# Kernel tuning notes

Measured on AMD Instinct MI355X. Metric: run time of the kernel, lower is better.

The kernel has to match this reference:

```python
import jax, jax.numpy as jnp
import numpy as np

EPS = 1e-5

def _ln(x, g, b):
    mu = jnp.mean(x, axis=-1, keepdims=True)
    var = jnp.mean(jnp.square(x - mu), axis=-1, keepdims=True)
    return (x - mu) * jax.lax.rsqrt(var + EPS) * g + b

def setup_inputs() -> dict:
    key = jax.random.key(0)
    ks = jax.random.split(key, 16)
    B, L, D, H = 1, 512, 128, 128  # d_pair=128, d_hidden=128
    s_d = 1.0 / np.sqrt(D)
    s_h = 1.0 / np.sqrt(H)
    return {
        "pair": jax.random.normal(ks[0], (B, L, L, D), jnp.float32),
        "ln_g": jnp.ones((D,), jnp.float32),
        "ln_b": jnp.zeros((D,), jnp.float32),
        "lw": jax.random.normal(ks[1], (H, D), jnp.float32) * s_d,
        "lb": jnp.zeros((H,), jnp.float32),
        "lgw": jax.random.normal(ks[2], (H, D), jnp.float32) * s_d,
        "lgb": jnp.ones((H,), jnp.float32),
        "rw": jax.random.normal(ks[3], (H, D), jnp.float32) * s_d,
        "rb": jnp.zeros((H,), jnp.float32),
        "rgw": jax.random.normal(ks[4], (H, D), jnp.float32) * s_d,
        "rgb": jnp.ones((H,), jnp.float32),
        "gw": jax.random.normal(ks[5], (D, D), jnp.float32) * s_d,
        "gb": jnp.ones((D,), jnp.float32),
        "lno_g": jnp.ones((H,), jnp.float32),
        "lno_b": jnp.zeros((H,), jnp.float32),
        "ow": jax.random.normal(ks[6], (D, H), jnp.float32) * s_h,
        "ob": jnp.zeros((D,), jnp.float32),
    }

def reference(pair, ln_g, ln_b, lw, lb, lgw, lgb, rw, rb, rgw, rgb, gw, gb, lno_g, lno_b, ow, ob):
    L = pair.shape[1]
    p = _ln(pair, ln_g, ln_b)                                   # [B,L,L,D]
    left = jax.nn.sigmoid(p @ lgw.T + lgb) * (p @ lw.T + lb)    # [B,L,L,H]
    right = jax.nn.sigmoid(p @ rgw.T + rgb) * (p @ rw.T + rb)   # [B,L,L,H]
    # outgoing: contract over k (second seq dim)
    out = jnp.einsum('bikd,bjkd->bijd', left, right / jnp.float32(L))
    out = _ln(out, lno_g, lno_b)
    out = out @ ow.T + ob                                       # [B,L,L,D]
    gate = jax.nn.sigmoid(p @ gw.T + gb)
    return gate * out
```

## Files before the change

kernel.cpp:

```cpp
#include <hip/hip_runtime.h>
#include <hip/hip_bf16.h>
#include <stdint.h>

#define LSEQ 512
#define LL   262144

typedef __attribute__((ext_vector_type(8))) short short8;
typedef __attribute__((ext_vector_type(4))) float f32x4;
typedef __attribute__((ext_vector_type(4))) unsigned short us4;
typedef __attribute__((ext_vector_type(8))) unsigned short us8;

static_assert(sizeof(short8) == 16, "");
static_assert(sizeof(us8) == 16, "");

__device__ inline unsigned short f2bf(float f){
  unsigned u = __builtin_bit_cast(unsigned, f);
  unsigned r = (u + 0x7fffu + ((u >> 16) & 1u)) >> 16;
  return (unsigned short)r;
}
__device__ inline float bf2f(unsigned short s){
  return __builtin_bit_cast(float, ((unsigned)s) << 16);
}
__device__ inline float sigm(float x){ return 1.f / (1.f + __expf(-x)); }

__device__ inline int sw256(int row, int byte_in_row){
  return row*256 + ((((byte_in_row >> 4) ^ (row & 7))) << 4) + (byte_in_row & 15);
}
__device__ inline int sw128(int row, int byte_in_row){
  return row*128 + ((((byte_in_row >> 4) ^ (row & 7))) << 4) + (byte_in_row & 15);
}

__device__ inline void gload16(const void* g, void* lds){
  __builtin_amdgcn_global_load_lds(
      (const __attribute__((address_space(1))) unsigned*)g,
      (__attribute__((address_space(3))) unsigned*)lds, 16, 0, 0);
}

__global__ __launch_bounds__(128) void k0_prep(
    const float* __restrict__ lw, const float* __restrict__ lgw,
    const float* __restrict__ rw, const float* __restrict__ rgw,
    const float* __restrict__ gw, const float* __restrict__ ow,
    const float* __restrict__ lnog, const float* __restrict__ lnob,
    const float* __restrict__ ob,
    unsigned short* __restrict__ wbf, float* __restrict__ swg, float* __restrict__ swb)
{
  const int dd = blockIdx.x;
  const int t  = threadIdx.x;
  const int idx = dd*128 + t;
  wbf[0*16384 + idx] = f2bf(lgw[idx]);
  wbf[1*16384 + idx] = f2bf(lw[idx]);
  wbf[2*16384 + idx] = f2bf(rgw[idx]);
  wbf[3*16384 + idx] = f2bf(rw[idx]);
  wbf[4*16384 + idx] = f2bf(gw[idx]);
  float o = ow[idx];
  float a = o * lnog[t];
  float b = o * lnob[t];
  wbf[5*16384 + idx] = f2bf(a);
  #pragma unroll
  for (int m = 1; m < 64; m <<= 1){ a += __shfl_xor(a, m); b += __shfl_xor(b, m); }
  __shared__ float sA[2], sB[2];
  if ((t & 63) == 0){ sA[t >> 6] = a; sB[t >> 6] = b; }
  __syncthreads();
  if (t == 0){ swg[dd] = sA[0] + sA[1]; swb[dd] = sB[0] + sB[1] + ob[dd]; }
}

__global__ __launch_bounds__(256) void k1_proj(
    const float* __restrict__ pair, const float* __restrict__ ln_g, const float* __restrict__ ln_b,
    const float* __restrict__ lb,  const float* __restrict__ lgb,
    const float* __restrict__ rb,  const float* __restrict__ rgb,
    const float* __restrict__ gb,
    const unsigned short* __restrict__ wbf,
    unsigned short* __restrict__ lt, unsigned short* __restrict__ rt,
    unsigned short* __restrict__ gate)
{
  __shared__ char p_l[32768];
  __shared__ char wb_l[32768];
  const int t = threadIdx.x;
  const int b = blockIdx.x;
  const int w = t >> 6, l = t & 63;
  const long pos0 = (long)(b >> 2)*512 + (long)(b & 3)*128;

  {
    const int col = (t & 31) * 4;
    const float4 g4 = *(const float4*)(ln_g + col);
    const float4 b4 = *(const float4*)(ln_b + col);
    #pragma unroll 4
    for (int pass = 0; pass < 16; ++pass){
      const int row = pass*8 + (t >> 5);
      const float4 x = *(const float4*)(pair + (pos0 + row)*128 + col);
      float s = x.x + x.y + x.z + x.w;
      float q = x.x*x.x + x.y*x.y + x.z*x.z + x.w*x.w;
      #pragma unroll
      for (int m = 1; m < 32; m <<= 1){ s += __shfl_xor(s, m); q += __shfl_xor(q, m); }
      const float mu = s * (1.f/128.f);
      const float rs = rsqrtf(q * (1.f/128.f) - mu*mu + 1e-5f);
      us4 o;
      o.x = f2bf((x.x - mu)*rs*g4.x + b4.x);
      o.y = f2bf((x.y - mu)*rs*g4.y + b4.y);
      o.z = f2bf((x.z - mu)*rs*g4.z + b4.z);
      o.w = f2bf((x.w - mu)*rs*g4.w + b4.w);
      *(us4*)(p_l + sw256(row, col*2)) = o;
    }
  }
  __syncthreads();

  auto stageW = [&](int wi){
    const char* ws = (const char*)(wbf + wi*16384);
    #pragma unroll
    for (int q = 0; q < 8; ++q){
      int P = q*4096 + t*16;
      gload16(ws + sw256(P >> 8, P & 255), wb_l + P);
    }
  };

  auto zero2 = [&](f32x4 (&a)[2][8]){
    #pragma unroll
    for (int m = 0; m < 2; ++m)
      #pragma unroll
      for (int n = 0; n < 8; ++n) a[m][n] = f32x4{0.f,0.f,0.f,0.f};
  };

  auto gemm = [&](f32x4 (&acc)[2][8]){
    #pragma unroll
    for (int ks = 0; ks < 4; ++ks){
      short8 a[2];
      #pragma unroll
      for (int m = 0; m < 2; ++m){
        int row = w*32 + m*16 + (l & 15);
        a[m] = *(const short8*)(p_l + sw256(row, ks*64 + (l >> 4)*16));
      }
      #pragma unroll
      for (int n = 0; n < 8; ++n){
        int row = n*16 + (l & 15);
        short8 bb = *(const short8*)(wb_l + sw256(row, ks*64 + (l >> 4)*16));
        #pragma unroll
        for (int m = 0; m < 2; ++m)
          acc[m][n] = __builtin_amdgcn_mfma_f32_16x16x32_bf16(a[m], bb, acc[m][n], 0, 0, 0);
      }
    }
  };

  auto combineWrite = [&](f32x4 (&aG)[2][8], f32x4 (&aL)[2][8],
                          const float* gbias, const float* lbias, unsigned short* dst){
    float gv[8], lv[8];
    #pragma unroll
    for (int n = 0; n < 8; ++n){ gv[n] = gbias[n*16 + (l & 15)]; lv[n] = lbias[n*16 + (l & 15)]; }
    __syncthreads();
    #pragma unroll
    for (int m = 0; m < 2; ++m){
      #pragma unroll
      for (int n = 0; n < 8; ++n){
        us4 o;
        #pragma unroll
        for (int r = 0; r < 4; ++r)
          o[r] = f2bf(sigm(aG[m][n][r] + gv[n]) * (aL[m][n][r] + lv[n]));
        int h  = n*16 + (l & 15);
        int r0 = w*32 + m*16 + (l >> 4)*4;
        *(us4*)(wb_l + sw256(h, r0*2)) = o;
      }
    }
    __syncthreads();
    #pragma unroll
    for (int it = 0; it < 8; ++it){
      int hh = it*16 + (t >> 4), ch = t & 15;
      us8 v = *(const us8*)(wb_l + sw256(hh, ch*16));
      *(us8*)(dst + (long)hh*LL + pos0 + ch*8) = v;
    }
    __syncthreads();
  };

  f32x4 aG[2][8], aL[2][8];

  zero2(aG); zero2(aL);
  stageW(0); __syncthreads(); gemm(aG); __syncthreads();
  stageW(1); __syncthreads(); gemm(aL);
  combineWrite(aG, aL, lgb, lb, lt);

  zero2(aG); zero2(aL);
  stageW(2); __syncthreads(); gemm(aG); __syncthreads();
  stageW(3); __syncthreads(); gemm(aL);
  combineWrite(aG, aL, rgb, rb, rt);

  zero2(aG);
  stageW(4); __syncthreads(); gemm(aG);
  {
    float gv[8];
    #pragma unroll
    for (int n = 0; n < 8; ++n) gv[n] = gb[n*16 + (l & 15)];
    __syncthreads();
    #pragma unroll
    for (int m = 0; m < 2; ++m)
      #pragma unroll
      for (int n = 0; n < 8; ++n)
        #pragma unroll
        for (int r = 0; r < 4; ++r){
          int row = w*32 + m*16 + (l >> 4)*4 + r;
          int h   = n*16 + (l & 15);
          *(unsigned short*)(wb_l + sw256(row, h*2)) = f2bf(sigm(aG[m][n][r] + gv[n]));
        }
    __syncthreads();
    #pragma unroll
    for (int it = 0; it < 8; ++it){
      int row = it*16 + (t >> 4), ch = t & 15;
      us8 v = *(const us8*)(wb_l + sw256(row, ch*16));
      *(us8*)(gate + (pos0 + row)*128 + ch*8) = v;
    }
  }
}

__global__ __launch_bounds__(256) void k2_tri(
    const unsigned short* __restrict__ lt, const unsigned short* __restrict__ rt,
    unsigned short* __restrict__ omm)
{
  __shared__ char smem[32768];
  char* As = smem;
  char* Bs = smem + 16384;
  const int t = threadIdx.x, b = blockIdx.x;
  const int d = b & 127, tile = b >> 7;
  const int i0 = (tile >> 2)*128, j0 = (tile & 3)*128;
  const unsigned short* Ag = lt + (long)d*LL;
  const unsigned short* Bg = rt + (long)d*LL;
  const int w = t >> 6, l = t & 63;
  const int wm = w >> 1, wn = w & 1;

  f32x4 acc[4][4];
  #pragma unroll
  for (int m = 0; m < 4; ++m)
    #pragma unroll
    for (int n = 0; n < 4; ++n) acc[m][n] = f32x4{0.f,0.f,0.f,0.f};

  for (int kt = 0; kt < 8; ++kt){
    const int k0 = kt*64;
    __syncthreads();
    #pragma unroll
    for (int q = 0; q < 4; ++q){
      int P = q*4096 + t*16;
      int row = P >> 7;
      int ls  = ((P >> 4) & 7) ^ (row & 7);
      gload16(Ag + (long)(i0 + row)*512 + k0 + ls*8, As + P);
      gload16(Bg + (long)(j0 + row)*512 + k0 + ls*8, Bs + P);
    }
    __syncthreads();
    #pragma unroll
    for (int ks = 0; ks < 2; ++ks){
      short8 a[4], bb[4];
      #pragma unroll
      for (int m = 0; m < 4; ++m){
        int row = wm*64 + m*16 + (l & 15);
        a[m] = *(const short8*)(As + sw128(row, ks*64 + (l >> 4)*16));
      }
      #pragma unroll
      for (int n = 0; n < 4; ++n){
        int row = wn*64 + n*16 + (l & 15);
        bb[n] = *(const short8*)(Bs + sw128(row, ks*64 + (l >> 4)*16));
      }
      #pragma unroll
      for (int m = 0; m < 4; ++m)
        #pragma unroll
        for (int n = 0; n < 4; ++n)
          acc[m][n] = __builtin_amdgcn_mfma_f32_16x16x32_bf16(a[m], bb[n], acc[m][n], 0, 0, 0);
    }
  }
  __syncthreads();
  #pragma unroll
  for (int m = 0; m < 4; ++m)
    #pragma unroll
    for (int n = 0; n < 4; ++n)
      #pragma unroll
      for (int r = 0; r < 4; ++r){
        int row = wm*64 + m*16 + (l >> 4)*4 + r;
        int j   = wn*64 + n*16 + (l & 15);
        *(unsigned short*)(smem + sw256(row, j*2)) = f2bf(acc[m][n][r] * (1.f/512.f));
      }
  __syncthreads();
  #pragma unroll
  for (int it = 0; it < 8; ++it){
    int row = it*16 + (t >> 4), ch = t & 15;
    us8 v = *(const us8*)(smem + sw256(row, ch*16));
    *(us8*)(omm + (long)d*LL + (long)(i0 + row)*512 + j0 + ch*8) = v;
  }
}

__global__ __launch_bounds__(256) void k3_out(
    const unsigned short* __restrict__ omm, const unsigned short* __restrict__ gate,
    const unsigned short* __restrict__ wgbf,
    const float* __restrict__ swg, const float* __restrict__ swb,
    float* __restrict__ out)
{
  __shared__ char omm_l[32768];
  __shared__ char wg_l[32768];
  __shared__ float mu_s[128], rs_s[128];
  const int t = threadIdx.x;
  const int jt = blockIdx.x, i = blockIdx.y;
  const int j0 = jt*128;
  const int w = t >> 6, l = t & 63;

  {
    const int jc = t & 15, dg = t >> 4;
    float sum[8], sq[8];
    #pragma unroll
    for (int e = 0; e < 8; ++e){ sum[e] = 0.f; sq[e] = 0.f; }
    #pragma unroll
    for (int q = 0; q < 8; ++q){
      int dd = dg + q*16;
      us8 v = *(const us8*)(omm + (long)dd*LL + (long)i*512 + j0 + jc*8);
      *(us8*)(omm_l + dd*256 + jc*16) = v;
      #pragma unroll
      for (int e = 0; e < 8; ++e){
        float f = bf2f(v[e]);
        sum[e] += f; sq[e] += f*f;
      }
    }
    float* scr = (float*)wg_l;
    #pragma unroll
    for (int e = 0; e < 8; ++e){
      scr[dg*128 + jc*8 + e]        = sum[e];
      scr[2048 + dg*128 + jc*8 + e] = sq[e];
    }
  }
  __syncthreads();
  if (t < 128){
    const float* scr = (const float*)wg_l;
    float s1 = 0.f, s2 = 0.f;
    #pragma unroll
    for (int g = 0; g < 16; ++g){ s1 += scr[g*128 + t]; s2 += scr[2048 + g*128 + t]; }
    float mu = s1 * (1.f/128.f);
    float var = s2 * (1.f/128.f) - mu*mu;
    mu_s[t] = mu;
    rs_s[t] = rsqrtf(var + 1e-5f);
  }
  __syncthreads();
  #pragma unroll
  for (int q = 0; q < 8; ++q){
    int P = q*4096 + t*16;
    gload16((const char*)wgbf + sw256(P >> 8, P & 255), wg_l + P);
  }
  __syncthreads();

  f32x4 acc[2][8];
  #pragma unroll
  for (int m = 0; m < 2; ++m)
    #pragma unroll
    for (int n = 0; n < 8; ++n) acc[m][n] = f32x4{0.f,0.f,0.f,0.f};

  #pragma unroll
  for (int ks = 0; ks < 4; ++ks){
    short8 a[2];
    #pragma unroll
    for (int m = 0; m < 2; ++m){
      const int jj = w*32 + m*16 + (l & 15);
      short8 av;
      #pragma unroll
      for (int e = 0; e < 8; ++e){
        int dd = ks*32 + (l >> 4)*8 + e;
        av[e] = *(const short*)(omm_l + dd*256 + jj*2);
      }
      a[m] = av;
    }
    #pragma unroll
    for (int n = 0; n < 8; ++n){
      int row = n*16 + (l & 15);
      short8 bb = *(const short8*)(wg_l + sw256(row, ks*64 + (l >> 4)*16));
      #pragma unroll
      for (int m = 0; m < 2; ++m)
        acc[m][n] = __builtin_amdgcn_mfma_f32_16x16x32_bf16(a[m], bb, acc[m][n], 0, 0, 0);
    }
  }

  float swgv[8], swbv[8];
  #pragma unroll
  for (int n = 0; n < 8; ++n){ swgv[n] = swg[n*16 + (l & 15)]; swbv[n] = swb[n*16 + (l & 15)]; }
  #pragma unroll
  for (int m = 0; m < 2; ++m){
    #pragma unroll
    for (int r = 0; r < 4; ++r){
      int j = w*32 + m*16 + (l >> 4)*4 + r;
      float mu = mu_s[j], rs = rs_s[j];
      long rowoff = ((long)i*512 + j0 + j)*128;
      #pragma unroll
      for (int n = 0; n < 8; ++n){
        int ddx = n*16 + (l & 15);
        float val = rs*(acc[m][n][r] - mu*swgv[n]) + swbv[n];
        out[rowoff + ddx] = val * bf2f(gate[rowoff + ddx]);
      }
    }
  }
}

extern "C" void kernel_launch(void* const* d_in, const int* in_sizes, int n_in,
                              void* d_out, int out_size, void* d_ws, size_t ws_size,
                              hipStream_t stream)
{
  const float* pair = (const float*)d_in[0];
  const float* ln_g = (const float*)d_in[1];
  const float* ln_b = (const float*)d_in[2];
  const float* lw   = (const float*)d_in[3];
  const float* lb   = (const float*)d_in[4];
  const float* lgw  = (const float*)d_in[5];
  const float* lgb  = (const float*)d_in[6];
  const float* rw   = (const float*)d_in[7];
  const float* rb   = (const float*)d_in[8];
  const float* rgw  = (const float*)d_in[9];
  const float* rgb  = (const float*)d_in[10];
  const float* gw   = (const float*)d_in[11];
  const float* gb   = (const float*)d_in[12];
  const float* lnog = (const float*)d_in[13];
  const float* lnob = (const float*)d_in[14];
  const float* ow   = (const float*)d_in[15];
  const float* ob   = (const float*)d_in[16];
  float* out = (float*)d_out;

  char* ws = (char*)d_ws;
  unsigned short* lt   = (unsigned short*)(ws);
  unsigned short* rt   = (unsigned short*)(ws + (1l << 26));
  unsigned short* gate = (unsigned short*)(ws + (2l << 26));
  unsigned short* omm  = (unsigned short*)(ws + (3l << 26));
  unsigned short* wbf  = (unsigned short*)(ws + (4l << 26));
  float* swg = (float*)(ws + (4l << 26) + 196608);
  float* swb = swg + 128;

  k0_prep<<<dim3(128), dim3(128), 0, stream>>>(lw, lgw, rw, rgw, gw, ow, lnog, lnob, ob,
                                               wbf, swg, swb);
  k1_proj<<<dim3(2048), dim3(256), 0, stream>>>(pair, ln_g, ln_b, lb, lgb, rb, rgb, gb,
                                                wbf, lt, rt, gate);
  k2_tri<<<dim3(2048), dim3(256), 0, stream>>>(lt, rt, omm);
  k3_out<<<dim3(4, 512), dim3(256), 0, stream>>>(omm, gate, wbf + 5*16384, swg, swb, out);
}
```

Before: 341.1 us.

## Pre-pack projection weights in MFMA fragment order and halve k1 tile size

Adds a pack kernel that lays out the five projection weight matrices in per-lane MFMA B-fragment order, so k1 loads them straight from global into registers instead of staging them through LDS. k1 now processes 64 rows per block and keeps the A fragments resident in registers. Each wave owns a slice of output columns and computes the gate and linear arms together. LDS use is halved and launch bounds request 3 blocks per CU to raise occupancy. The packed weights live in the omm workspace region, which k2 overwrites only later. The trade-off is that weights are re-read from global/L2 by every block, and there is more register pressure from holding the A fragments.

```diff
diff --git a/kernel.cpp b/kernel.cpp
--- a/kernel.cpp
+++ b/kernel.cpp
@@ -37,25 +37,17 @@
 }
 
 __global__ __launch_bounds__(128) void k0_prep(
-    const float* __restrict__ lw, const float* __restrict__ lgw,
-    const float* __restrict__ rw, const float* __restrict__ rgw,
-    const float* __restrict__ gw, const float* __restrict__ ow,
-    const float* __restrict__ lnog, const float* __restrict__ lnob,
-    const float* __restrict__ ob,
-    unsigned short* __restrict__ wbf, float* __restrict__ swg, float* __restrict__ swb)
+    const float* __restrict__ ow, const float* __restrict__ lnog,
+    const float* __restrict__ lnob, const float* __restrict__ ob,
+    unsigned short* __restrict__ wgbf, float* __restrict__ swg, float* __restrict__ swb)
 {
   const int dd = blockIdx.x;
   const int t  = threadIdx.x;
   const int idx = dd*128 + t;
-  wbf[0*16384 + idx] = f2bf(lgw[idx]);
-  wbf[1*16384 + idx] = f2bf(lw[idx]);
-  wbf[2*16384 + idx] = f2bf(rgw[idx]);
-  wbf[3*16384 + idx] = f2bf(rw[idx]);
-  wbf[4*16384 + idx] = f2bf(gw[idx]);
   float o = ow[idx];
   float a = o * lnog[t];
   float b = o * lnob[t];
-  wbf[5*16384 + idx] = f2bf(a);
+  wgbf[idx] = f2bf(a);
   #pragma unroll
   for (int m = 1; m < 64; m <<= 1){ a += __shfl_xor(a, m); b += __shfl_xor(b, m); }
   __shared__ float sA[2], sB[2];
@@ -64,28 +56,43 @@
   if (t == 0){ swg[dd] = sA[0] + sA[1]; swb[dd] = sB[0] + sB[1] + ob[dd]; }
 }
 
-__global__ __launch_bounds__(256) void k1_proj(
+__global__ __launch_bounds__(64) void kP_pack(
+    const float* __restrict__ lgw, const float* __restrict__ lw,
+    const float* __restrict__ rgw, const float* __restrict__ rw,
+    const float* __restrict__ gw, short8* __restrict__ wpk)
+{
+  const int b = blockIdx.x;
+  const int arm = b >> 5, n = (b >> 2) & 7, ks = b & 3;
+  const float* src = arm==0 ? lgw : arm==1 ? lw : arm==2 ? rgw : arm==3 ? rw : gw;
+  const int l = threadIdx.x;
+  const int h = n*16 + (l & 15), k0 = ks*32 + (l >> 4)*8;
+  short8 v;
+  #pragma unroll
+  for (int e = 0; e < 8; ++e) v[e] = (short)f2bf(src[h*128 + k0 + e]);
+  wpk[b*64 + l] = v;
+}
+
+__global__ __launch_bounds__(256, 3) void k1_proj(
     const float* __restrict__ pair, const float* __restrict__ ln_g, const float* __restrict__ ln_b,
     const float* __restrict__ lb,  const float* __restrict__ lgb,
     const float* __restrict__ rb,  const float* __restrict__ rgb,
     const float* __restrict__ gb,
-    const unsigned short* __restrict__ wbf,
+    const short8* __restrict__ wpk,
     unsigned short* __restrict__ lt, unsigned short* __restrict__ rt,
     unsigned short* __restrict__ gate)
 {
-  __shared__ char p_l[32768];
-  __shared__ char wb_l[32768];
+  __shared__ char p_l[16384];
+  __shared__ char epi[16384];
   const int t = threadIdx.x;
-  const int b = blockIdx.x;
   const int w = t >> 6, l = t & 63;
-  const long pos0 = (long)(b >> 2)*512 + (long)(b & 3)*128;
+  const long pos0 = (long)blockIdx.x * 64;
 
   {
     const int col = (t & 31) * 4;
     const float4 g4 = *(const float4*)(ln_g + col);
     const float4 b4 = *(const float4*)(ln_b + col);
-    #pragma unroll 4
-    for (int pass = 0; pass < 16; ++pass){
+    #pragma unroll
+    for (int pass = 0; pass < 8; ++pass){
       const int row = pass*8 + (t >> 5);
       const float4 x = *(const float4*)(pair + (pos0 + row)*128 + col);
       float s = x.x + x.y + x.z + x.w;
@@ -104,105 +111,105 @@
   }
   __syncthreads();
 
-  auto stageW = [&](int wi){
-    const char* ws = (const char*)(wbf + wi*16384);
-    #pragma unroll
-    for (int q = 0; q < 8; ++q){
-      int P = q*4096 + t*16;
-      gload16(ws + sw256(P >> 8, P & 255), wb_l + P);
-    }
+  short8 a[4][4];
+  #pragma unroll
+  for (int m = 0; m < 4; ++m)
+    #pragma unroll
+    for (int ks = 0; ks < 4; ++ks)
+      a[m][ks] = *(const short8*)(p_l + sw256(m*16 + (l & 15), ks*64 + (l >> 4)*16));
+
+  auto zero42 = [&](f32x4 (&acc)[4][2]){
+    #pragma unroll
+    for (int m = 0; m < 4; ++m){ acc[m][0] = f32x4{0,0,0,0}; acc[m][1] = f32x4{0,0,0,0}; }
   };
 
-  auto zero2 = [&](f32x4 (&a)[2][8]){
-    #pragma unroll
-    for (int m = 0; m < 2; ++m)
-      #pragma unroll
-      for (int n = 0; n < 8; ++n) a[m][n] = f32x4{0.f,0.f,0.f,0.f};
+  auto gemm2 = [&](int armG, int armL, f32x4 (&aG)[4][2], f32x4 (&aL)[4][2]){
+    #pragma unroll
+    for (int n2 = 0; n2 < 2; ++n2){
+      const int n = w*2 + n2;
+      short8 bg[4], blv[4];
+      #pragma unroll
+      for (int ks = 0; ks < 4; ++ks){
+        bg[ks]  = wpk[((armG*8 + n)*4 + ks)*64 + l];
+        blv[ks] = wpk[((armL*8 + n)*4 + ks)*64 + l];
+      }
+      #pragma unroll
+      for (int ks = 0; ks < 4; ++ks)
+        #pragma unroll
+        for (int m = 0; m < 4; ++m){
+          aG[m][n2] = __builtin_amdgcn_mfma_f32_16x16x32_bf16(a[m][ks], bg[ks],  aG[m][n2], 0, 0, 0);
+          aL[m][n2] = __builtin_amdgcn_mfma_f32_16x16x32_bf16(a[m][ks], blv[ks], aL[m][n2], 0, 0, 0);
+        }
+    }
   };
 
-  auto gemm = [&](f32x4 (&acc)[2][8]){
-    #pragma unroll
-    for (int ks = 0; ks < 4; ++ks){
-      short8 a[2];
-      #pragma unroll
-      for (int m = 0; m < 2; ++m){
-        int row = w*32 + m*16 + (l & 15);
-        a[m] = *(const short8*)(p_l + sw256(row, ks*64 + (l >> 4)*16));
-      }
-      #pragma unroll
-      for (int n = 0; n < 8; ++n){
-        int row = n*16 + (l & 15);
-        short8 bb = *(const short8*)(wb_l + sw256(row, ks*64 + (l >> 4)*16));
-        #pragma unroll
-        for (int m = 0; m < 2; ++m)
-          acc[m][n] = __builtin_amdgcn_mfma_f32_16x16x32_bf16(a[m], bb, acc[m][n], 0, 0, 0);
-      }
-    }
-  };
-
-  auto combineWrite = [&](f32x4 (&aG)[2][8], f32x4 (&aL)[2][8],
-                          const float* gbias, const float* lbias, unsigned short* dst){
-    float gv[8], lv[8];
-    #pragma unroll
-    for (int n = 0; n < 8; ++n){ gv[n] = gbias[n*16 + (l & 15)]; lv[n] = lbias[n*16 + (l & 15)]; }
-    __syncthreads();
-    #pragma unroll
-    for (int m = 0; m < 2; ++m){
-      #pragma unroll
-      for (int n = 0; n < 8; ++n){
+  auto epiT = [&](f32x4 (&aG)[4][2], f32x4 (&aL)[4][2],
+                  const float* __restrict__ gbias, const float* __restrict__ lbias,
+                  unsigned short* __restrict__ dst){
+    #pragma unroll
+    for (int n2 = 0; n2 < 2; ++n2){
+      const int h = w*32 + n2*16 + (l & 15);
+      const float gv = gbias[h], lv = lbias[h];
+      #pragma unroll
+      for (int m = 0; m < 4; ++m){
         us4 o;
         #pragma unroll
         for (int r = 0; r < 4; ++r)
-          o[r] = f2bf(sigm(aG[m][n][r] + gv[n]) * (aL[m][n][r] + lv[n]));
-        int h  = n*16 + (l & 15);
-        int r0 = w*32 + m*16 + (l >> 4)*4;
-        *(us4*)(wb_l + sw256(h, r0*2)) = o;
+          o[r] = f2bf(sigm(aG[m][n2][r] + gv) * (aL[m][n2][r] + lv));
+        *(us4*)(epi + sw128(h, (m*16 + (l >> 4)*4)*2)) = o;
       }
     }
     __syncthreads();
     #pragma unroll
-    for (int it = 0; it < 8; ++it){
-      int hh = it*16 + (t >> 4), ch = t & 15;
-      us8 v = *(const us8*)(wb_l + sw256(hh, ch*16));
+    for (int p = 0; p < 4; ++p){
+      const int hh = p*32 + (t >> 3), ch = t & 7;
+      us8 v = *(const us8*)(epi + sw128(hh, ch*16));
       *(us8*)(dst + (long)hh*LL + pos0 + ch*8) = v;
     }
     __syncthreads();
   };
 
-  f32x4 aG[2][8], aL[2][8];
-
-  zero2(aG); zero2(aL);
-  stageW(0); __syncthreads(); gemm(aG); __syncthreads();
-  stageW(1); __syncthreads(); gemm(aL);
-  combineWrite(aG, aL, lgb, lb, lt);
-
-  zero2(aG); zero2(aL);
-  stageW(2); __syncthreads(); gemm(aG); __syncthreads();
-  stageW(3); __syncthreads(); gemm(aL);
-  combineWrite(aG, aL, rgb, rb, rt);
-
-  zero2(aG);
-  stageW(4); __syncthreads(); gemm(aG);
+  f32x4 aG[4][2], aL[4][2];
+
+  zero42(aG); zero42(aL);
+  gemm2(0, 1, aG, aL);
+  epiT(aG, aL, lgb, lb, lt);
+
+  zero42(aG); zero42(aL);
+  gemm2(2, 3, aG, aL);
+  epiT(aG, aL, rgb, rb, rt);
+
+  zero42(aG);
+  #pragma unroll
+  for (int n2 = 0; n2 < 2; ++n2){
+    const int n = w*2 + n2;
+    short8 bg[4];
+    #pragma unroll
+    for (int ks = 0; ks < 4; ++ks) bg[ks] = wpk[((4*8 + n)*4 + ks)*64 + l];
+    #pragma unroll
+    for (int ks = 0; ks < 4; ++ks)
+      #pragma unroll
+      for (int m = 0; m < 4; ++m)
+        aG[m][n2] = __builtin_amdgcn_mfma_f32_16x16x32_bf16(a[m][ks], bg[ks], aG[m][n2], 0, 0, 0);
+  }
   {
-    float gv[8];
-    #pragma unroll
-    for (int n = 0; n < 8; ++n) gv[n] = gb[n*16 + (l & 15)];
-    __syncthreads();
-    #pragma unroll
-    for (int m = 0; m < 2; ++m)
-      #pragma unroll
-      for (int n = 0; n < 8; ++n)
+    #pragma unroll
+    for (int n2 = 0; n2 < 2; ++n2){
+      const int h = w*32 + n2*16 + (l & 15);
+      const float gv = gb[h];
+      #pragma unroll
+      for (int m = 0; m < 4; ++m)
         #pragma unroll
         for (int r = 0; r < 4; ++r){
-          int row = w*32 + m*16 + (l >> 4)*4 + r;
-          int h   = n*16 + (l & 15);
-          *(unsigned short*)(wb_l + sw256(row, h*2)) = f2bf(sigm(aG[m][n][r] + gv[n]));
+          const int pos = m*16 + (l >> 4)*4 + r;
+          *(unsigned short*)(epi + sw256(pos, h*2)) = f2bf(sigm(aG[m][n2][r] + gv));
         }
+    }
     __syncthreads();
     #pragma unroll
-    for (int it = 0; it < 8; ++it){
-      int row = it*16 + (t >> 4), ch = t & 15;
-      us8 v = *(const us8*)(wb_l + sw256(row, ch*16));
+    for (int p = 0; p < 4; ++p){
+      const int row = p*16 + (t >> 4), ch = t & 15;
+      us8 v = *(const us8*)(epi + sw256(row, ch*16));
       *(us8*)(gate + (pos0 + row)*128 + ch*8) = v;
     }
   }
@@ -415,14 +422,15 @@
   unsigned short* rt   = (unsigned short*)(ws + (1l << 26));
   unsigned short* gate = (unsigned short*)(ws + (2l << 26));
   unsigned short* omm  = (unsigned short*)(ws + (3l << 26));
-  unsigned short* wbf  = (unsigned short*)(ws + (4l << 26));
-  float* swg = (float*)(ws + (4l << 26) + 196608);
+  short8*         wpk  = (short8*)(ws + (3l << 26));
+  unsigned short* wgbf = (unsigned short*)(ws + (4l << 26));
+  float* swg = (float*)(ws + (4l << 26) + 65536);
   float* swb = swg + 128;
 
-  k0_prep<<<dim3(128), dim3(128), 0, stream>>>(lw, lgw, rw, rgw, gw, ow, lnog, lnob, ob,
-                                               wbf, swg, swb);
-  k1_proj<<<dim3(2048), dim3(256), 0, stream>>>(pair, ln_g, ln_b, lb, lgb, rb, rgb, gb,
-                                                wbf, lt, rt, gate);
+  k0_prep<<<dim3(128), dim3(128), 0, stream>>>(ow, lnog, lnob, ob, wgbf, swg, swb);
+  kP_pack<<<dim3(160), dim3(64), 0, stream>>>(lgw, lw, rgw, rw, gw, wpk);
+  k1_proj<<<dim3(4096), dim3(256), 0, stream>>>(pair, ln_g, ln_b, lb, lgb, rb, rgb, gb,
+                                                wpk, lt, rt, gate);
   k2_tri<<<dim3(2048), dim3(256), 0, stream>>>(lt, rt, omm);
-  k3_out<<<dim3(4, 512), dim3(256), 0, stream>>>(omm, gate, wbf + 5*16384, swg, swb, out);
-}
+  k3_out<<<dim3(4, 512), dim3(256), 0, stream>>>(omm, gate, wgbf, swg, swb, out);
+}
```

Result: faster. 297.9 us (-12.7%).
